# Performance work log

Hardware: AMD Instinct MI355X
Metric: run time of the kernel (lower is better)

The kernel has to match this reference:

```python
import jax, jax.numpy as jnp
import numpy as np

ITERS = 3
EPS = 1e-6


def setup_inputs() -> dict:
    key = jax.random.key(0)
    k1, k2 = jax.random.split(key, 2)
    a = jax.random.normal(k1, (64, 1152, 1, 1, 1, 1), dtype=jnp.float32)
    v = jax.random.normal(k2, (64, 1152, 32, 4, 4, 1), dtype=jnp.float32)
    logits = jnp.ones((1, 1152, 32, 1, 1, 1), dtype=jnp.float32)
    return {"a": a, "v": v, "logits": logits}


def _squash(s):
    # s: (batch, 1, B, P, P, 1); norm over dim 2 (matches torch code, dim=2)
    norm_sq = jnp.sum(s * s, axis=2, keepdims=True)
    return jnp.sqrt(norm_sq + EPS) / (1.0 + norm_sq) * s


def reference(a, v, logits):
    # a: (batch, A, 1, 1, 1, 1) -- unused (overwritten in original forward)
    # v: (batch, A, B, P, P, 1); logits: (1, A, B, 1, 1, 1)
    batch = v.shape[0]
    b = jnp.broadcast_to(logits, (batch,) + logits.shape[1:])
    p = None
    for i in range(ITERS):
        c = jax.nn.softmax(b, axis=2)                    # route over B
        s = jnp.sum(c * v, axis=1, keepdims=True)        # (batch,1,B,P,P,1)
        p = _squash(s)
        if i < ITERS - 1:
            # agreement: sum over pose dims -> (batch, A, B, 1, 1, 1)
            b = b + jnp.sum(p * v, axis=(-3, -2, -1), keepdims=True)
    p = jnp.squeeze(p, axis=1)                           # (batch, B, P, P, 1)
    a_out = jnp.linalg.norm(p, ord=2, axis=2)            # (batch, B, P, 1)
    return (a_out, p)
```

## Files before the change

kernel.cpp:

```cpp
#include <hip/hip_runtime.h>
#include <math.h>

#define BATCH 64
#define ADIM  1152
#define BDIM  32
#define POSE  16
#define SLICE 512
#define CHUNKS 16
#define A_PER_CHUNK 72
#define STEPS 9
#define EPSQ 1e-6f
#define SPART_ITER ((size_t)BATCH * CHUNKS * SLICE)

template<int ITER>
__global__ __launch_bounds__(256) void route_pass(
    const float* __restrict__ v,
    const float* __restrict__ logits,
    const float* __restrict__ s_part,
    float* __restrict__ s_out)
{
    const int bt    = blockIdx.x / CHUNKS;
    const int chunk = blockIdx.x % CHUNKS;
    const int t     = threadIdx.x;
    const int bc    = t & 31;
    const int a_sub = t >> 5;

    __shared__ __align__(16) float smem[8 * SLICE];
    __shared__ float sred[SLICE];
    __shared__ float fac[POSE];
    float4* tile = (float4*)smem;

    float p0[POSE], p1[POSE];
#pragma unroll
    for (int j = 0; j < ITER; ++j) {
        for (int e = t; e < SLICE; e += 256) {
            const float* sp = s_part + (size_t)j * SPART_ITER
                            + (size_t)bt * CHUNKS * SLICE + e;
            float s = 0.f;
#pragma unroll
            for (int c = 0; c < CHUNKS; ++c) s += sp[c * SLICE];
            sred[e] = s;
        }
        __syncthreads();
        if (t < POSE) {
            float ns = 0.f;
            for (int b2 = 0; b2 < BDIM; ++b2) {
                float x = sred[b2 * POSE + t];
                ns += x * x;
            }
            fac[t] = sqrtf(ns + EPSQ) / (1.f + ns);
        }
        __syncthreads();
#pragma unroll
        for (int k = 0; k < POSE; ++k) {
            float pv = fac[k] * sred[bc * POSE + k];
            if (j == 0) p0[k] = pv; else p1[k] = pv;
        }
        __syncthreads();
    }

    float acc[POSE];
#pragma unroll
    for (int k = 0; k < POSE; ++k) acc[k] = 0.f;

    const int a0 = chunk * A_PER_CHUNK;
    const float4* gbase = (const float4*)(v + ((size_t)bt * ADIM + a0) * SLICE);

    float4 r0 = gbase[t];
    float4 r1 = gbase[t + 256];
    float4 r2 = gbase[t + 512];
    float4 r3 = gbase[t + 768];

    for (int step = 0; step < STEPS; ++step) {
        {
            int L, row, col;
            L = t;        row = L >> 7; col = L & 127; tile[row*128 + (col ^ ((col>>2)&7))] = r0;
            L = t + 256;  row = L >> 7; col = L & 127; tile[row*128 + (col ^ ((col>>2)&7))] = r1;
            L = t + 512;  row = L >> 7; col = L & 127; tile[row*128 + (col ^ ((col>>2)&7))] = r2;
            L = t + 768;  row = L >> 7; col = L & 127; tile[row*128 + (col ^ ((col>>2)&7))] = r3;
        }
        __syncthreads();

        if (step + 1 < STEPS) {
            const float4* gnext = gbase + (size_t)(step + 1) * 1024;
            r0 = gnext[t];
            r1 = gnext[t + 256];
            r2 = gnext[t + 512];
            r3 = gnext[t + 768];
        }

        float vv[POSE];
#pragma unroll
        for (int q = 0; q < 4; ++q) {
            float4 f = tile[a_sub * 128 + ((bc * 4 + q) ^ (bc & 7))];
            vv[4*q+0] = f.x; vv[4*q+1] = f.y; vv[4*q+2] = f.z; vv[4*q+3] = f.w;
        }

        const int a = a0 + step * 8 + a_sub;
        float bval = logits[a * BDIM + bc];
        if (ITER >= 1) {
            float d = 0.f;
#pragma unroll
            for (int k = 0; k < POSE; ++k) d = fmaf(p0[k], vv[k], d);
            bval += d;
        }
        if (ITER >= 2) {
            float d = 0.f;
#pragma unroll
            for (int k = 0; k < POSE; ++k) d = fmaf(p1[k], vv[k], d);
            bval += d;
        }

        float m = bval;
#pragma unroll
        for (int off = 16; off > 0; off >>= 1)
            m = fmaxf(m, __shfl_xor(m, off, 32));
        float e = __expf(bval - m);
        float ssum = e;
#pragma unroll
        for (int off = 16; off > 0; off >>= 1)
            ssum += __shfl_xor(ssum, off, 32);
        float c = e / ssum;

#pragma unroll
        for (int k = 0; k < POSE; ++k) acc[k] = fmaf(c, vv[k], acc[k]);
        __syncthreads();
    }

    float* red = smem;
#pragma unroll
    for (int k = 0; k < POSE; ++k) red[a_sub * SLICE + bc * POSE + k] = acc[k];
    __syncthreads();

    for (int idx = t; idx < SLICE; idx += 256) {
        float s = 0.f;
#pragma unroll
        for (int asb = 0; asb < 8; ++asb) s += red[asb * SLICE + idx];
        s_out[((size_t)bt * CHUNKS + chunk) * SLICE + idx] = s;
    }
}

__global__ __launch_bounds__(512) void final_out(
    const float* __restrict__ s_part2,
    float* __restrict__ out)
{
    const int bt = blockIdx.x;
    const int t  = threadIdx.x;
    const int pose = t & 15;

    __shared__ float sq[512];
    __shared__ float ns[16];

    float sv = 0.f;
#pragma unroll
    for (int c = 0; c < CHUNKS; ++c)
        sv += s_part2[((size_t)bt * CHUNKS + c) * SLICE + t];

    sq[t] = sv * sv;
    __syncthreads();
    if (t < 16) {
        float a = 0.f;
        for (int b2 = 0; b2 < BDIM; ++b2) a += sq[b2 * POSE + t];
        ns[t] = a;
    }
    __syncthreads();
    float n = ns[pose];
    float pv = sqrtf(n + EPSQ) / (1.f + n) * sv;

    out[8192 + bt * SLICE + t] = pv;
    sq[t] = pv * pv;
    __syncthreads();
    if (t < 128) {
        int b2 = t >> 2, p2 = t & 3;
        float a = 0.f;
#pragma unroll
        for (int p1 = 0; p1 < 4; ++p1) a += sq[b2 * POSE + p1 * 4 + p2];
        out[bt * 128 + b2 * 4 + p2] = sqrtf(a);
    }
}

extern "C" void kernel_launch(void* const* d_in, const int* in_sizes, int n_in,
                              void* d_out, int out_size, void* d_ws, size_t ws_size,
                              hipStream_t stream) {
    const float* v      = (const float*)d_in[1];
    const float* logits = (const float*)d_in[2];
    float* out = (float*)d_out;

    float* s_part = (float*)d_ws;

    route_pass<0><<<dim3(BATCH * CHUNKS), dim3(256), 0, stream>>>(
        v, logits, s_part, s_part + 0 * SPART_ITER);
    route_pass<1><<<dim3(BATCH * CHUNKS), dim3(256), 0, stream>>>(
        v, logits, s_part, s_part + 1 * SPART_ITER);
    route_pass<2><<<dim3(BATCH * CHUNKS), dim3(256), 0, stream>>>(
        v, logits, s_part, s_part + 2 * SPART_ITER);
    final_out<<<dim3(BATCH), dim3(512), 0, stream>>>(
        s_part + 2 * SPART_ITER, out);
}
```

Baseline: 275.6 us.

## Load v directly into registers with double buffering and hoist squash into separate kernel

Drops the shared-memory tile staging and per-step block barriers. Each wave now loads its own rows of v straight into registers, with a two-group double buffer so the next loads overlap the current compute. The squash of the previous iteration's partial sums moves into a small separate kernel, so every routing block no longer repeats that reduction. The chunk count drops from 16 to 12, and the softmax no longer subtracts the max. That removes shuffles but can overflow if the logits grow large.

```diff
diff --git a/kernel.cpp b/kernel.cpp
--- a/kernel.cpp
+++ b/kernel.cpp
@@ -6,9 +6,10 @@
 #define BDIM  32
 #define POSE  16
 #define SLICE 512
-#define CHUNKS 16
-#define A_PER_CHUNK 72
-#define STEPS 9
+#define CHUNKS 12
+#define ROWS_PER_CHUNK 96
+#define ROWS_PER_WAVE 24
+#define GROUPS 6
 #define EPSQ 1e-6f
 #define SPART_ITER ((size_t)BATCH * CHUNKS * SLICE)
 
@@ -16,128 +17,131 @@
 __global__ __launch_bounds__(256) void route_pass(
     const float* __restrict__ v,
     const float* __restrict__ logits,
-    const float* __restrict__ s_part,
+    const float* __restrict__ p_buf,
     float* __restrict__ s_out)
 {
     const int bt    = blockIdx.x / CHUNKS;
     const int chunk = blockIdx.x % CHUNKS;
     const int t     = threadIdx.x;
-    const int bc    = t & 31;
-    const int a_sub = t >> 5;
-
-    __shared__ __align__(16) float smem[8 * SLICE];
-    __shared__ float sred[SLICE];
-    __shared__ float fac[POSE];
-    float4* tile = (float4*)smem;
+    const int wv    = t >> 6;
+    const int lane  = t & 63;
+    const int bc    = lane & 31;
+    const int a_sub = lane >> 5;
 
     float p0[POSE], p1[POSE];
-#pragma unroll
-    for (int j = 0; j < ITER; ++j) {
-        for (int e = t; e < SLICE; e += 256) {
-            const float* sp = s_part + (size_t)j * SPART_ITER
-                            + (size_t)bt * CHUNKS * SLICE + e;
-            float s = 0.f;
-#pragma unroll
-            for (int c = 0; c < CHUNKS; ++c) s += sp[c * SLICE];
-            sred[e] = s;
-        }
-        __syncthreads();
-        if (t < POSE) {
-            float ns = 0.f;
-            for (int b2 = 0; b2 < BDIM; ++b2) {
-                float x = sred[b2 * POSE + t];
-                ns += x * x;
+    if (ITER >= 1) {
+        const float4* pp = (const float4*)(p_buf + (size_t)bt * SLICE + bc * POSE);
+#pragma unroll
+        for (int q = 0; q < 4; ++q) {
+            float4 f = pp[q];
+            p0[4*q+0]=f.x; p0[4*q+1]=f.y; p0[4*q+2]=f.z; p0[4*q+3]=f.w;
+        }
+    }
+    if (ITER >= 2) {
+        const float4* pp = (const float4*)(p_buf + (size_t)(BATCH + bt) * SLICE + bc * POSE);
+#pragma unroll
+        for (int q = 0; q < 4; ++q) {
+            float4 f = pp[q];
+            p1[4*q+0]=f.x; p1[4*q+1]=f.y; p1[4*q+2]=f.z; p1[4*q+3]=f.w;
+        }
+    }
+
+    float acc[POSE];
+#pragma unroll
+    for (int k = 0; k < POSE; ++k) acc[k] = 0.f;
+
+    const int row0 = chunk * ROWS_PER_CHUNK + wv * ROWS_PER_WAVE;
+    const float* base = v + ((size_t)bt * ADIM + row0) * SLICE;
+
+    float vA[2][POSE], vB[2][POSE];
+
+    auto load_group = [&](float (*dst)[POSE], int g) {
+#pragma unroll
+        for (int j = 0; j < 2; ++j) {
+            const float4* p4 = (const float4*)(base + (size_t)(g * 4 + 2 * j + a_sub) * SLICE + bc * POSE);
+#pragma unroll
+            for (int q = 0; q < 4; ++q) {
+                float4 f = p4[q];
+                dst[j][4*q+0]=f.x; dst[j][4*q+1]=f.y; dst[j][4*q+2]=f.z; dst[j][4*q+3]=f.w;
             }
-            fac[t] = sqrtf(ns + EPSQ) / (1.f + ns);
-        }
-        __syncthreads();
-#pragma unroll
-        for (int k = 0; k < POSE; ++k) {
-            float pv = fac[k] * sred[bc * POSE + k];
-            if (j == 0) p0[k] = pv; else p1[k] = pv;
-        }
-        __syncthreads();
-    }
-
-    float acc[POSE];
-#pragma unroll
-    for (int k = 0; k < POSE; ++k) acc[k] = 0.f;
-
-    const int a0 = chunk * A_PER_CHUNK;
-    const float4* gbase = (const float4*)(v + ((size_t)bt * ADIM + a0) * SLICE);
-
-    float4 r0 = gbase[t];
-    float4 r1 = gbase[t + 256];
-    float4 r2 = gbase[t + 512];
-    float4 r3 = gbase[t + 768];
-
-    for (int step = 0; step < STEPS; ++step) {
-        {
-            int L, row, col;
-            L = t;        row = L >> 7; col = L & 127; tile[row*128 + (col ^ ((col>>2)&7))] = r0;
-            L = t + 256;  row = L >> 7; col = L & 127; tile[row*128 + (col ^ ((col>>2)&7))] = r1;
-            L = t + 512;  row = L >> 7; col = L & 127; tile[row*128 + (col ^ ((col>>2)&7))] = r2;
-            L = t + 768;  row = L >> 7; col = L & 127; tile[row*128 + (col ^ ((col>>2)&7))] = r3;
-        }
-        __syncthreads();
-
-        if (step + 1 < STEPS) {
-            const float4* gnext = gbase + (size_t)(step + 1) * 1024;
-            r0 = gnext[t];
-            r1 = gnext[t + 256];
-            r2 = gnext[t + 512];
-            r3 = gnext[t + 768];
-        }
-
-        float vv[POSE];
-#pragma unroll
-        for (int q = 0; q < 4; ++q) {
-            float4 f = tile[a_sub * 128 + ((bc * 4 + q) ^ (bc & 7))];
-            vv[4*q+0] = f.x; vv[4*q+1] = f.y; vv[4*q+2] = f.z; vv[4*q+3] = f.w;
-        }
-
-        const int a = a0 + step * 8 + a_sub;
-        float bval = logits[a * BDIM + bc];
-        if (ITER >= 1) {
-            float d = 0.f;
-#pragma unroll
-            for (int k = 0; k < POSE; ++k) d = fmaf(p0[k], vv[k], d);
-            bval += d;
-        }
-        if (ITER >= 2) {
-            float d = 0.f;
-#pragma unroll
-            for (int k = 0; k < POSE; ++k) d = fmaf(p1[k], vv[k], d);
-            bval += d;
-        }
-
-        float m = bval;
-#pragma unroll
-        for (int off = 16; off > 0; off >>= 1)
-            m = fmaxf(m, __shfl_xor(m, off, 32));
-        float e = __expf(bval - m);
-        float ssum = e;
-#pragma unroll
-        for (int off = 16; off > 0; off >>= 1)
-            ssum += __shfl_xor(ssum, off, 32);
-        float c = e / ssum;
-
-#pragma unroll
-        for (int k = 0; k < POSE; ++k) acc[k] = fmaf(c, vv[k], acc[k]);
-        __syncthreads();
-    }
-
-    float* red = smem;
-#pragma unroll
-    for (int k = 0; k < POSE; ++k) red[a_sub * SLICE + bc * POSE + k] = acc[k];
+        }
+    };
+
+    auto compute_group = [&](float (*vv)[POSE], int g) {
+#pragma unroll
+        for (int j = 0; j < 2; ++j) {
+            const int a = row0 + g * 4 + 2 * j + a_sub;
+            float bval = logits[a * BDIM + bc];
+            if (ITER >= 1) {
+                float d = 0.f;
+#pragma unroll
+                for (int k = 0; k < POSE; ++k) d = fmaf(p0[k], vv[j][k], d);
+                bval += d;
+            }
+            if (ITER >= 2) {
+                float d = 0.f;
+#pragma unroll
+                for (int k = 0; k < POSE; ++k) d = fmaf(p1[k], vv[j][k], d);
+                bval += d;
+            }
+            float e = __expf(bval);
+            float ssum = e;
+#pragma unroll
+            for (int off = 16; off > 0; off >>= 1)
+                ssum += __shfl_xor(ssum, off, 32);
+            float c = e / ssum;
+#pragma unroll
+            for (int k = 0; k < POSE; ++k) acc[k] = fmaf(c, vv[j][k], acc[k]);
+        }
+    };
+
+    load_group(vA, 0);
+#pragma unroll
+    for (int g = 0; g < GROUPS; ++g) {
+        float (*cur)[POSE] = (g & 1) ? vB : vA;
+        float (*nxt)[POSE] = (g & 1) ? vA : vB;
+        if (g + 1 < GROUPS) load_group(nxt, g + 1);
+        compute_group(cur, g);
+    }
+
+    __shared__ float red[8 * SLICE];
+#pragma unroll
+    for (int k = 0; k < POSE; ++k)
+        red[(wv * 2 + a_sub) * SLICE + bc * POSE + k] = acc[k];
     __syncthreads();
 
     for (int idx = t; idx < SLICE; idx += 256) {
         float s = 0.f;
 #pragma unroll
-        for (int asb = 0; asb < 8; ++asb) s += red[asb * SLICE + idx];
+        for (int w = 0; w < 8; ++w) s += red[w * SLICE + idx];
         s_out[((size_t)bt * CHUNKS + chunk) * SLICE + idx] = s;
     }
+}
+
+__global__ __launch_bounds__(512) void squash_pass(
+    const float* __restrict__ s_part_j,
+    float* __restrict__ p_out_j)
+{
+    const int bt = blockIdx.x;
+    const int t  = threadIdx.x;
+
+    __shared__ float sq[SLICE];
+    __shared__ float fac[POSE];
+
+    float sv = 0.f;
+#pragma unroll
+    for (int c = 0; c < CHUNKS; ++c)
+        sv += s_part_j[((size_t)bt * CHUNKS + c) * SLICE + t];
+
+    sq[t] = sv * sv;
+    __syncthreads();
+    if (t < POSE) {
+        float n = 0.f;
+        for (int b2 = 0; b2 < BDIM; ++b2) n += sq[b2 * POSE + t];
+        fac[t] = sqrtf(n + EPSQ) / (1.f + n);
+    }
+    __syncthreads();
+    p_out_j[(size_t)bt * SLICE + t] = fac[t & 15] * sv;
 }
 
 __global__ __launch_bounds__(512) void final_out(
@@ -148,8 +152,8 @@
     const int t  = threadIdx.x;
     const int pose = t & 15;
 
-    __shared__ float sq[512];
-    __shared__ float ns[16];
+    __shared__ float sq[SLICE];
+    __shared__ float ns[POSE];
 
     float sv = 0.f;
 #pragma unroll
@@ -158,7 +162,7 @@
 
     sq[t] = sv * sv;
     __syncthreads();
-    if (t < 16) {
+    if (t < POSE) {
         float a = 0.f;
         for (int b2 = 0; b2 < BDIM; ++b2) a += sq[b2 * POSE + t];
         ns[t] = a;
@@ -187,13 +191,18 @@
     float* out = (float*)d_out;
 
     float* s_part = (float*)d_ws;
+    float* p_buf  = s_part + 3 * SPART_ITER;
 
     route_pass<0><<<dim3(BATCH * CHUNKS), dim3(256), 0, stream>>>(
-        v, logits, s_part, s_part + 0 * SPART_ITER);
+        v, logits, p_buf, s_part + 0 * SPART_ITER);
+    squash_pass<<<dim3(BATCH), dim3(512), 0, stream>>>(
+        s_part + 0 * SPART_ITER, p_buf);
     route_pass<1><<<dim3(BATCH * CHUNKS), dim3(256), 0, stream>>>(
-        v, logits, s_part, s_part + 1 * SPART_ITER);
+        v, logits, p_buf, s_part + 1 * SPART_ITER);
+    squash_pass<<<dim3(BATCH), dim3(512), 0, stream>>>(
+        s_part + 1 * SPART_ITER, p_buf + (size_t)BATCH * SLICE);
     route_pass<2><<<dim3(BATCH * CHUNKS), dim3(256), 0, stream>>>(
-        v, logits, s_part, s_part + 2 * SPART_ITER);
+        v, logits, p_buf, s_part + 2 * SPART_ITER);
     final_out<<<dim3(BATCH), dim3(512), 0, stream>>>(
         s_part + 2 * SPART_ITER, out);
 }
```

After: 323.7 us. 1.17x slower.
